# Kernel tuning notes

Measured on AMD Instinct MI355X. Metric: run time of the kernel, lower is better.

The kernel has to match this reference:

```python
import jax, jax.numpy as jnp
import numpy as np

B, S, D, H, HD = 8, 1374, 384, 6, 64
NUM_PATCHES = 1369  # (518 // 14) ** 2
NUM_PREFIX = 5      # 1 cls + 4 registers


def setup_inputs() -> dict:
    key = jax.random.key(0)
    ks = jax.random.split(key, 10)
    init = 0.02  # truncated_normal(0.02) approximated by scaled normal
    x = jax.random.normal(ks[0], (B, S, D), jnp.float32)
    wq = jax.random.truncated_normal(ks[1], -2.0, 2.0, (D, H, HD), jnp.float32) * init
    wk = jax.random.truncated_normal(ks[2], -2.0, 2.0, (D, H, HD), jnp.float32) * init
    wv = jax.random.truncated_normal(ks[3], -2.0, 2.0, (D, H, HD), jnp.float32) * init
    wo = jax.random.truncated_normal(ks[4], -2.0, 2.0, (H, HD, D), jnp.float32) * init
    bq = jnp.zeros((H, HD), jnp.float32)
    bk = jnp.zeros((H, HD), jnp.float32)
    bv = jnp.zeros((H, HD), jnp.float32)
    bo = jnp.zeros((D,), jnp.float32)
    keep_patch_indices = jax.random.randint(ks[5], (B, NUM_PATCHES), 0, NUM_PATCHES).astype(jnp.int64)
    return {"x": x, "wq": wq, "bq": bq, "wk": wk, "bk": bk, "wv": wv, "bv": bv,
            "wo": wo, "bo": bo, "keep_patch_indices": keep_patch_indices, "k_patches": 685}


def reference(x, wq, bq, wk, bk, wv, bv, wo, bo, keep_patch_indices, k_patches):
    # q/k/v projections: DenseGeneral to (heads, head_dim)
    q = jnp.einsum('bsd,dhe->bshe', x, wq) + bq
    k = jnp.einsum('bsd,dhe->bshe', x, wk) + bk
    v = jnp.einsum('bsd,dhe->bshe', x, wv) + bv

    z = jnp.einsum('bqhd,bkhd->bhqk', q / (HD ** 0.5), k)  # [B,H,S,S]
    attn_logits = z  # saved BEFORE masking (used by 'mse' criterion)

    # dynamic scatter mask: patch columns >= k_patches get -inf
    num_selected = keep_patch_indices.shape[1]
    patch_idx = jnp.arange(num_selected)
    indices_to_mask = jnp.where(patch_idx >= k_patches, patch_idx, num_selected) + NUM_PREFIX
    # out-of-bounds indices (== num_selected + NUM_PREFIX) are dropped by JAX scatter semantics
    z = z.at[:, :, :, indices_to_mask].set(-jnp.inf)

    attn_map = jax.nn.softmax(z, axis=-1)
    zo = jnp.einsum('bhqk,bkhd->bqhd', attn_map, v)
    output = jnp.einsum('bqhd,hdo->bqo', zo, wo) + bo  # wo contracts (heads, head_dim)

    # attn_aggregate = ['cls_token','reg_token','patch_token'], zoom_map_criterion='mse'
    am = attn_logits.mean(axis=1)  # mean over heads -> [B,S,S]
    aggs = jnp.stack([
        am[:, 0:1, :].mean(axis=1),      # cls token
        am[:, 1:5, :].mean(axis=1),      # register tokens
        am[:, 5:1374, :].mean(axis=1),   # patch tokens
    ], axis=1)                            # [B,3,S]
    attn_agg = aggs.mean(axis=1)          # [B,S]
    return output, attn_agg
```

## Files before the change

kernel.cpp:

```cpp
#include <hip/hip_runtime.h>
#include <stdint.h>

#define BB 8
#define SS 1374
#define DD 384
#define HH 6
#define HDIM 64
#define MROWS (BB*SS)
#define NPFX 5
#define SPAD 1376

typedef __attribute__((ext_vector_type(8))) short bf16x8;
typedef __attribute__((ext_vector_type(4))) float f32x4;
typedef __attribute__((ext_vector_type(2))) unsigned int u32x2;
typedef __attribute__((ext_vector_type(4))) unsigned int u32x4;
typedef u32x4 __attribute__((aligned(4))) u32x4_u;

__device__ __forceinline__ unsigned short f2bf(float f){
  union { float f; unsigned int u; } v; v.f = f;
  return (unsigned short)((v.u + 0x7FFFu + ((v.u >> 16) & 1u)) >> 16);
}
__device__ __forceinline__ float bf2f(unsigned short b){
  union { float f; unsigned int u; } v; v.u = ((unsigned int)b) << 16; return v.f;
}
__device__ __forceinline__ unsigned int pk_bf16(float a, float b){
#if __has_builtin(__builtin_amdgcn_cvt_pk_bf16_f32)
  typedef __attribute__((ext_vector_type(2))) __bf16 bfv2;
  bfv2 p = __builtin_amdgcn_cvt_pk_bf16_f32(a, b);
  union { bfv2 v; unsigned int u; } c; c.v = p; return c.u;
#else
  return (unsigned int)f2bf(a) | ((unsigned int)f2bf(b) << 16);
#endif
}

__global__ void k_conv_x(const float* __restrict__ x, unsigned short* __restrict__ xb, int n4){
  int i = blockIdx.x*blockDim.x + threadIdx.x;
  if (i >= n4) return;
  f32x4 v = *(const f32x4*)(x + (size_t)i*4);
  u32x2 o; o[0] = pk_bf16(v[0], v[1]); o[1] = pk_bf16(v[2], v[3]);
  *(u32x2*)(xb + (size_t)i*4) = o;
}

__global__ void k_conv_w(const float* __restrict__ wq, const float* __restrict__ wk,
                         const float* __restrict__ wv, const float* __restrict__ wo,
                         unsigned short* __restrict__ wbT, unsigned short* __restrict__ woT){
  int i = blockIdx.x*blockDim.x + threadIdx.x;
  if (i < 1152*384){
    int n = i / 384, d = i % 384;
    const float* w = (n < 384) ? wq : (n < 768) ? wk : wv;
    wbT[i] = f2bf(w[(size_t)d*384 + (n % 384)]);
  } else if (i < 1152*384 + 384*384){
    int j = i - 1152*384;
    int n = j / 384, k = j % 384;
    woT[j] = f2bf(wo[(size_t)k*384 + n]);
  }
}

__global__ void k_xbar(const float* __restrict__ x, float* __restrict__ xbar){
  int b = blockIdx.x / 11, ch = blockIdx.x % 11;
  int d = threadIdx.x;
  int s0 = ch*128, s1 = s0 + 128; if (s1 > SS) s1 = SS;
  float acc = 0.f;
  for (int s = s0; s < s1; ++s){
    float w = (s == 0) ? (1.f/3.f) : (s < 5) ? (1.f/12.f) : (1.f/4107.f);
    acc += w * x[((size_t)b*SS + s)*DD + d];
  }
  atomicAdd(&xbar[b*DD + d], acc);
}

__global__ void k_qbar(const float* __restrict__ xbar, const float* __restrict__ wq,
                       const float* __restrict__ bq, float* __restrict__ qbar){
  __shared__ float xs[DD];
  int b = blockIdx.x, t = threadIdx.x;
  xs[t] = xbar[b*DD + t];
  __syncthreads();
  float acc = bq[t];
  for (int d = 0; d < DD; ++d) acc += xs[d]*wq[(size_t)d*384 + t];
  qbar[b*384 + t] = acc;
}

__global__ void k_agg(const float* __restrict__ qbar, const unsigned short* __restrict__ kg,
                      float* __restrict__ out_agg){
  __shared__ float qs[384];
  int b = blockIdx.x / 6, sb = blockIdx.x % 6;
  int t = threadIdx.x;
  for (int i = t; i < 384; i += 256) qs[i] = qbar[b*384 + i];
  __syncthreads();
  int s = sb*256 + t;
  if (s >= SS) return;
  float acc = 0.f;
  for (int h = 0; h < HH; ++h){
    const unsigned short* kr = kg + (((size_t)(b*HH + h))*SS + s)*64;
    const float* qh = qs + h*64;
    for (int c = 0; c < 8; ++c){
      u32x4 v = *(const u32x4*)(kr + c*8);
      #pragma unroll
      for (int j = 0; j < 4; ++j){
        unsigned int u = v[j];
        acc += qh[c*8 + 2*j]     * bf2f((unsigned short)(u & 0xFFFFu));
        acc += qh[c*8 + 2*j + 1] * bf2f((unsigned short)(u >> 16));
      }
    }
  }
  out_agg[b*SS + s] = acc * (1.f/48.f);
}

template<int MODE>
__global__ __launch_bounds__(256) void k_gemm(
    const unsigned short* __restrict__ A, const unsigned short* __restrict__ Bt,
    const float* __restrict__ b0, const float* __restrict__ b1, const float* __restrict__ b2,
    unsigned short* __restrict__ qg, unsigned short* __restrict__ kgp,
    unsigned short* __restrict__ vt, float* __restrict__ out)
{
  int mt = blockIdx.x % 86, nt = blockIdx.x / 86;
  const int t = threadIdx.x;
  const int w = t >> 6, lane = t & 63, quad = lane >> 4, l16 = lane & 15;
  const int wm = w >> 1, wn = w & 1;
  constexpr int SMEM_SH = (MODE==0) ? 13824 : 17408;
  __shared__ unsigned short smem[SMEM_SH];
  unsigned short* As = smem;
  unsigned short* Bs = smem + 9216;
  f32x4 acc[4][2];
  #pragma unroll
  for (int i=0;i<4;i++){ acc[i][0] = (f32x4){0,0,0,0}; acc[i][1] = (f32x4){0,0,0,0}; }
  const int m0 = mt*128, n0 = nt*64;

  const int ar = t >> 1, akb = (t & 1) * 32;
  int ga = m0 + ar; if (ga > MROWS-1) ga = MROWS-1;
  const unsigned short* ap = A + (size_t)ga*384 + akb;
  const int br = t >> 2, bkb = (t & 3) * 16;
  const unsigned short* bp = Bt + (size_t)(n0 + br)*384 + bkb;

  u32x4 ra[4], rb[2];
  #pragma unroll
  for (int i=0;i<4;i++) ra[i] = *(const u32x4*)(ap + i*8);
  rb[0] = *(const u32x4*)(bp); rb[1] = *(const u32x4*)(bp + 8);

  for (int kc = 0; kc < 6; ++kc){
    __syncthreads();
    #pragma unroll
    for (int i=0;i<4;i++) *(u32x4*)(As + ar*72 + akb + i*8) = ra[i];
    *(u32x4*)(Bs + br*72 + bkb)     = rb[0];
    *(u32x4*)(Bs + br*72 + bkb + 8) = rb[1];
    __syncthreads();
    if (kc + 1 < 6){
      int kn = (kc+1)*64;
      #pragma unroll
      for (int i=0;i<4;i++) ra[i] = *(const u32x4*)(ap + kn + i*8);
      rb[0] = *(const u32x4*)(bp + kn); rb[1] = *(const u32x4*)(bp + kn + 8);
    }
    #pragma unroll
    for (int kh = 0; kh < 2; ++kh){
      bf16x8 af[4], bfr[2];
      #pragma unroll
      for (int rf = 0; rf < 4; ++rf)
        af[rf] = *(const bf16x8*)(As + (wm*64 + rf*16 + l16)*72 + kh*32 + quad*8);
      #pragma unroll
      for (int cf = 0; cf < 2; ++cf)
        bfr[cf] = *(const bf16x8*)(Bs + (wn*32 + cf*16 + l16)*72 + kh*32 + quad*8);
      #pragma unroll
      for (int rf = 0; rf < 4; ++rf)
        #pragma unroll
        for (int cf = 0; cf < 2; ++cf)
          acc[rf][cf] = __builtin_amdgcn_mfma_f32_16x16x32_bf16(af[rf], bfr[cf], acc[rf][cf], 0,0,0);
    }
  }

  const int b0r = m0 / SS, s0r = m0 % SS;
  __syncthreads();
  if (MODE == 1){
    float* CsF = (float*)smem;
    #pragma unroll
    for (int cf = 0; cf < 2; ++cf){
      int e = wn*32 + cf*16 + l16;
      float bias = b0[n0 + e];
      #pragma unroll
      for (int rf = 0; rf < 4; ++rf){
        int rr = wm*64 + rf*16 + quad*4;
        #pragma unroll
        for (int r4 = 0; r4 < 4; ++r4)
          CsF[(rr + r4)*68 + e] = acc[rf][cf][r4] + bias;
      }
    }
    __syncthreads();
    #pragma unroll
    for (int p = 0; p < 8; ++p){
      int r = p*16 + (t >> 4), c = t & 15;
      int rr = m0 + r;
      if (rr < MROWS){
        f32x4 v = *(const f32x4*)(CsF + r*68 + c*4);
        *(f32x4*)(out + (size_t)rr*384 + n0 + c*4) = v;
      }
    }
  } else {
    const int mat = nt / 6, h = nt - mat*6;
    const float* bvp = (mat==0) ? b0 : (mat==1) ? b1 : b2;
    const float vsc = (mat==0) ? 0.125f : 1.f;
    if (mat < 2){
      unsigned short* Cs = As;
      unsigned short* dst = (mat==0) ? qg : kgp;
      #pragma unroll
      for (int cf = 0; cf < 2; ++cf){
        int e = wn*32 + cf*16 + l16;
        float bias = bvp[h*64 + e];
        #pragma unroll
        for (int rf = 0; rf < 4; ++rf){
          int rr = wm*64 + rf*16 + quad*4;
          #pragma unroll
          for (int r4 = 0; r4 < 4; ++r4)
            Cs[(rr + r4)*72 + e] = f2bf((acc[rf][cf][r4] + bias)*vsc);
        }
      }
      __syncthreads();
      #pragma unroll
      for (int p = 0; p < 4; ++p){
        int r = p*32 + (t >> 3), c = t & 7;
        int rr = m0 + r;
        if (rr < MROWS){
          int s = s0r + r, bb = b0r;
          if (s >= SS){ s -= SS; ++bb; }
          u32x4 v = *(const u32x4*)(Cs + r*72 + c*8);
          *(u32x4*)(dst + (((size_t)(bb*HH + h))*SS + s)*64 + c*8) = v;
        }
      }
    } else {
      unsigned short* CsV = As;
      #pragma unroll
      for (int cf = 0; cf < 2; ++cf){
        int e = wn*32 + cf*16 + l16;
        float bias = bvp[h*64 + e];
        #pragma unroll
        for (int rf = 0; rf < 4; ++rf){
          int rr = wm*64 + rf*16 + quad*4;
          #pragma unroll
          for (int p = 0; p < 2; ++p)
            *(unsigned int*)(CsV + e*136 + rr + p*2) =
                pk_bf16(acc[rf][cf][p*2] + bias, acc[rf][cf][p*2+1] + bias);
        }
      }
      __syncthreads();
      const bool nowrap = (s0r + 127 < SS) && (m0 + 127 < MROWS);
      if (nowrap){
        int e = t >> 2;
        unsigned short* vrow = vt + ((size_t)(b0r*HH + h)*64 + e)*SPAD + s0r;
        #pragma unroll
        for (int i = 0; i < 4; ++i){
          int c = (t & 3)*4 + i;
          u32x4 v = *(const u32x4*)(CsV + e*136 + c*8);
          *(u32x4_u*)(vrow + c*8) = v;
        }
      } else {
        for (int idx = t; idx < 64*64; idx += 256){
          int e = idx >> 6, sp = (idx & 63)*2;
          int rr = m0 + sp;
          if (rr < MROWS){
            int s = s0r + sp, bb = b0r;
            if (s >= SS){ s -= SS; ++bb; }
            *(unsigned int*)(vt + ((size_t)(bb*HH + h)*64 + e)*SPAD + s) =
                *(const unsigned int*)(CsV + e*136 + sp);
          }
        }
      }
    }
  }
}

#define KSTR 72
__global__ __launch_bounds__(256) void k_attn(
    const unsigned short* __restrict__ qg, const unsigned short* __restrict__ kg,
    const unsigned short* __restrict__ vt, unsigned short* __restrict__ zo,
    const int* __restrict__ kpat)
{
  const int QB = (SS + 63)/64;
  int qb = blockIdx.x % QB, bh = blockIdx.x / QB;
  int t = threadIdx.x, w = t >> 6, lane = t & 63, quad = lane >> 4, l16 = lane & 15;
  int SK = NPFX + kpat[0]; if (SK > SS) SK = SS; if (SK < 1) SK = 1;
  int niter = (SK + 63) >> 6;
  __shared__ unsigned short Ks[64*KSTR];
  __shared__ unsigned short Vs[64*KSTR];
  __shared__ unsigned short Ps[4*16*KSTR];
  int q0 = qb*64 + w*16;
  bf16x8 aq[2];
  {
    int qrow = q0 + l16;
    if (qrow < SS){
      const unsigned short* p = qg + ((size_t)bh*SS + qrow)*64;
      aq[0] = *(const bf16x8*)(p + quad*8);
      aq[1] = *(const bf16x8*)(p + 32 + quad*8);
    } else {
      bf16x8 z8 = {0,0,0,0,0,0,0,0};
      aq[0] = z8; aq[1] = z8;
    }
  }
  f32x4 o[4];
  #pragma unroll
  for (int i=0;i<4;i++) o[i] = (f32x4){0.f,0.f,0.f,0.f};
  float rsum[4] = {0.f,0.f,0.f,0.f};

  const int srow = t >> 2, sc = t & 3;
  const unsigned short* kbase = kg + ((size_t)bh*SS)*64;
  const unsigned short* vbase = vt + ((size_t)bh*64)*SPAD;
  u32x4 rk0, rk1, rv0, rv1;
  rk0 = *(const u32x4*)(kbase + (size_t)srow*64 + sc*8);
  rk1 = *(const u32x4*)(kbase + (size_t)srow*64 + (sc+4)*8);
  rv0 = *(const u32x4*)(vbase + (size_t)srow*SPAD + sc*8);
  rv1 = *(const u32x4*)(vbase + (size_t)srow*SPAD + (sc+4)*8);

  for (int it = 0; it < niter; ++it){
    int k0 = it*64;
    __syncthreads();
    *(u32x4*)(Ks + srow*KSTR + sc*8)     = rk0;
    *(u32x4*)(Ks + srow*KSTR + (sc+4)*8) = rk1;
    *(u32x4*)(Vs + srow*KSTR + sc*8)     = rv0;
    *(u32x4*)(Vs + srow*KSTR + (sc+4)*8) = rv1;
    __syncthreads();
    if (it + 1 < niter){
      int kn = k0 + 64;
      rk0 = *(const u32x4*)(kbase + (size_t)(kn + srow)*64 + sc*8);
      rk1 = *(const u32x4*)(kbase + (size_t)(kn + srow)*64 + (sc+4)*8);
      rv0 = *(const u32x4*)(vbase + (size_t)srow*SPAD + kn + sc*8);
      rv1 = *(const u32x4*)(vbase + (size_t)srow*SPAD + kn + (sc+4)*8);
    }
    float p[2][2][4];
    bool tail = (k0 + 64 > SK);
    #pragma unroll
    for (int h = 0; h < 2; ++h){
      #pragma unroll
      for (int ns = 0; ns < 2; ++ns){
        f32x4 zf = (f32x4){0.f,0.f,0.f,0.f};
        #pragma unroll
        for (int ec = 0; ec < 2; ++ec){
          bf16x8 bkf = *(const bf16x8*)(Ks + (h*32 + 2*l16 + ns)*KSTR + ec*32 + quad*8);
          zf = __builtin_amdgcn_mfma_f32_16x16x32_bf16(aq[ec], bkf, zf, 0,0,0);
        }
        bool valid = !tail || (k0 + h*32 + 2*l16 + ns) < SK;
        #pragma unroll
        for (int rg = 0; rg < 4; ++rg) p[h][ns][rg] = valid ? __expf(zf[rg]) : 0.f;
      }
    }
    unsigned short* Pw = Ps + w*16*KSTR;
    #pragma unroll
    for (int rg = 0; rg < 4; ++rg){
      rsum[rg] += (p[0][0][rg] + p[0][1][rg]) + (p[1][0][rg] + p[1][1][rg]);
      *(unsigned int*)(Pw + (quad*4+rg)*KSTR      + 2*l16) = pk_bf16(p[0][0][rg], p[0][1][rg]);
      *(unsigned int*)(Pw + (quad*4+rg)*KSTR + 32 + 2*l16) = pk_bf16(p[1][0][rg], p[1][1][rg]);
    }
    #pragma unroll
    for (int kc = 0; kc < 2; ++kc){
      bf16x8 ap = *(const bf16x8*)(Pw + l16*KSTR + kc*32 + quad*8);
      #pragma unroll
      for (int nc = 0; nc < 4; ++nc){
        bf16x8 bvf = *(const bf16x8*)(Vs + (nc*16 + l16)*KSTR + kc*32 + quad*8);
        o[nc] = __builtin_amdgcn_mfma_f32_16x16x32_bf16(ap, bvf, o[nc], 0,0,0);
      }
    }
  }
  #pragma unroll
  for (int rg = 0; rg < 4; ++rg){
    float s = rsum[rg];
    #pragma unroll
    for (int off = 8; off >= 1; off >>= 1) s += __shfl_xor(s, off);
    rsum[rg] = s;
  }
  int b = bh / HH, h = bh % HH;
  #pragma unroll
  for (int rg = 0; rg < 4; ++rg){
    int q = q0 + quad*4 + rg;
    if (q >= SS) continue;
    float inv = 1.f / rsum[rg];
    unsigned short* dst = zo + ((size_t)b*SS + q)*384 + h*64;
    #pragma unroll
    for (int nc = 0; nc < 4; ++nc) dst[nc*16 + l16] = f2bf(o[nc][rg]*inv);
  }
}

extern "C" void kernel_launch(void* const* d_in, const int* in_sizes, int n_in,
                              void* d_out, int out_size, void* d_ws, size_t ws_size,
                              hipStream_t stream){
  const float* x  = (const float*)d_in[0];
  const float* wq = (const float*)d_in[1];
  const float* bq = (const float*)d_in[2];
  const float* wk = (const float*)d_in[3];
  const float* bk = (const float*)d_in[4];
  const float* wv = (const float*)d_in[5];
  const float* bv = (const float*)d_in[6];
  const float* wo = (const float*)d_in[7];
  const float* bo = (const float*)d_in[8];
  const int* kpat = (const int*)d_in[10];
  float* out = (float*)d_out;
  float* out_agg = out + (size_t)MROWS*DD;

  char* ws = (char*)d_ws;
  unsigned short* xb  = (unsigned short*)(ws);
  unsigned short* wbT = (unsigned short*)(ws +  8441856);
  unsigned short* woT = (unsigned short*)(ws +  9326592);
  unsigned short* qg  = (unsigned short*)(ws +  9621504);
  unsigned short* kg  = (unsigned short*)(ws + 18063360);
  unsigned short* vt  = (unsigned short*)(ws + 26505216);
  unsigned short* zo  = (unsigned short*)(ws + 34959360);
  float* xbar         = (float*)(ws + 43401216);
  float* qbar         = (float*)(ws + 43413504);
  (void)in_sizes; (void)n_in; (void)out_size; (void)ws_size;

  hipMemsetAsync(xbar, 0, BB*DD*sizeof(float), stream);
  k_conv_x<<<(MROWS*DD/4 + 255)/256, 256, 0, stream>>>(x, xb, MROWS*DD/4);
  k_conv_w<<<((1152*384 + 384*384) + 255)/256, 256, 0, stream>>>(wq, wk, wv, wo, wbT, woT);
  k_xbar<<<BB*11, DD, 0, stream>>>(x, xbar);
  k_qbar<<<BB, DD, 0, stream>>>(xbar, wq, bq, qbar);
  k_gemm<0><<<86*18, 256, 0, stream>>>(xb, wbT, bq, bk, bv, qg, kg, vt, nullptr);
  k_attn<<<BB*HH*22, 256, 0, stream>>>(qg, kg, vt, zo, kpat);
  k_agg<<<BB*6, 256, 0, stream>>>(qbar, kg, out_agg);
  k_gemm<1><<<86*6, 256, 0, stream>>>(zo, woT, bo, nullptr, nullptr, nullptr, nullptr, nullptr, out);
}
```

Measured before the change: 212.3 us.

## Fuse x conversion with xbar reduction; restructure attention to per-wave tiles without LDS staging

The x-to-bf16 conversion and the weighted xbar reduction now run in one kernel, so x is read from global memory once instead of twice. The attention kernel no longer stages K/V tiles through shared memory with block-wide barriers. Each wave handles 32 query rows as two 16-row fragments and loads K and V fragments straight from global memory, reusing each fragment across both query fragments. This removes the __syncthreads overhead and doubles register-level reuse per load. The cost is more global/L2 traffic per wave, since the four waves in a block no longer share K/V, and the scalar per-element bf16 stores in the fused prep kernel may be less efficient than the old vectorized conversion.

```diff
diff --git a/kernel.cpp b/kernel.cpp
--- a/kernel.cpp
+++ b/kernel.cpp
@@ -33,12 +33,19 @@
 #endif
 }
 
-__global__ void k_conv_x(const float* __restrict__ x, unsigned short* __restrict__ xb, int n4){
-  int i = blockIdx.x*blockDim.x + threadIdx.x;
-  if (i >= n4) return;
-  f32x4 v = *(const f32x4*)(x + (size_t)i*4);
-  u32x2 o; o[0] = pk_bf16(v[0], v[1]); o[1] = pk_bf16(v[2], v[3]);
-  *(u32x2*)(xb + (size_t)i*4) = o;
+__global__ void k_prep_x(const float* __restrict__ x, unsigned short* __restrict__ xb,
+                         float* __restrict__ xbar){
+  int b = blockIdx.x / 43, ch = blockIdx.x % 43;
+  int d = threadIdx.x;
+  int s0 = ch*32, s1 = s0 + 32; if (s1 > SS) s1 = SS;
+  float acc = 0.f;
+  for (int s = s0; s < s1; ++s){
+    float v = x[((size_t)b*SS + s)*DD + d];
+    float w = (s == 0) ? (1.f/3.f) : (s < 5) ? (1.f/12.f) : (1.f/4107.f);
+    acc += w * v;
+    xb[((size_t)b*SS + s)*DD + d] = f2bf(v);
+  }
+  atomicAdd(&xbar[b*DD + d], acc);
 }
 
 __global__ void k_conv_w(const float* __restrict__ wq, const float* __restrict__ wk,
@@ -54,18 +61,6 @@
     int n = j / 384, k = j % 384;
     woT[j] = f2bf(wo[(size_t)k*384 + n]);
   }
-}
-
-__global__ void k_xbar(const float* __restrict__ x, float* __restrict__ xbar){
-  int b = blockIdx.x / 11, ch = blockIdx.x % 11;
-  int d = threadIdx.x;
-  int s0 = ch*128, s1 = s0 + 128; if (s1 > SS) s1 = SS;
-  float acc = 0.f;
-  for (int s = s0; s < s1; ++s){
-    float w = (s == 0) ? (1.f/3.f) : (s < 5) ? (1.f/12.f) : (1.f/4107.f);
-    acc += w * x[((size_t)b*SS + s)*DD + d];
-  }
-  atomicAdd(&xbar[b*DD + d], acc);
 }
 
 __global__ void k_qbar(const float* __restrict__ xbar, const float* __restrict__ wq,
@@ -265,112 +260,96 @@
   }
 }
 
-#define KSTR 72
 __global__ __launch_bounds__(256) void k_attn(
     const unsigned short* __restrict__ qg, const unsigned short* __restrict__ kg,
     const unsigned short* __restrict__ vt, unsigned short* __restrict__ zo,
     const int* __restrict__ kpat)
 {
-  const int QB = (SS + 63)/64;
-  int qb = blockIdx.x % QB, bh = blockIdx.x / QB;
   int t = threadIdx.x, w = t >> 6, lane = t & 63, quad = lane >> 4, l16 = lane & 15;
+  int wid = blockIdx.x*4 + w;
+  int bh = wid / 43, qt = wid - bh*43;
+  int q0 = qt*32;
   int SK = NPFX + kpat[0]; if (SK > SS) SK = SS; if (SK < 1) SK = 1;
   int niter = (SK + 63) >> 6;
-  __shared__ unsigned short Ks[64*KSTR];
-  __shared__ unsigned short Vs[64*KSTR];
-  __shared__ unsigned short Ps[4*16*KSTR];
-  int q0 = qb*64 + w*16;
-  bf16x8 aq[2];
-  {
-    int qrow = q0 + l16;
-    if (qrow < SS){
-      const unsigned short* p = qg + ((size_t)bh*SS + qrow)*64;
-      aq[0] = *(const bf16x8*)(p + quad*8);
-      aq[1] = *(const bf16x8*)(p + 32 + quad*8);
-    } else {
-      bf16x8 z8 = {0,0,0,0,0,0,0,0};
-      aq[0] = z8; aq[1] = z8;
-    }
-  }
-  f32x4 o[4];
-  #pragma unroll
-  for (int i=0;i<4;i++) o[i] = (f32x4){0.f,0.f,0.f,0.f};
-  float rsum[4] = {0.f,0.f,0.f,0.f};
-
-  const int srow = t >> 2, sc = t & 3;
+  __shared__ unsigned short Ps[4][32*72];
+  unsigned short* Pw = &Ps[w][0];
   const unsigned short* kbase = kg + ((size_t)bh*SS)*64;
   const unsigned short* vbase = vt + ((size_t)bh*64)*SPAD;
-  u32x4 rk0, rk1, rv0, rv1;
-  rk0 = *(const u32x4*)(kbase + (size_t)srow*64 + sc*8);
-  rk1 = *(const u32x4*)(kbase + (size_t)srow*64 + (sc+4)*8);
-  rv0 = *(const u32x4*)(vbase + (size_t)srow*SPAD + sc*8);
-  rv1 = *(const u32x4*)(vbase + (size_t)srow*SPAD + (sc+4)*8);
+
+  bf16x8 aq[2][2];
+  #pragma unroll
+  for (int qf = 0; qf < 2; ++qf){
+    int qrow = q0 + qf*16 + l16; if (qrow > SS-1) qrow = SS-1;
+    const unsigned short* p = qg + ((size_t)bh*SS + qrow)*64;
+    aq[qf][0] = *(const bf16x8*)(p + quad*8);
+    aq[qf][1] = *(const bf16x8*)(p + 32 + quad*8);
+  }
+  f32x4 o[2][4];
+  #pragma unroll
+  for (int qf=0;qf<2;qf++)
+    #pragma unroll
+    for (int nc=0;nc<4;nc++) o[qf][nc] = (f32x4){0.f,0.f,0.f,0.f};
+  float rsum[2][4] = {{0.f,0.f,0.f,0.f},{0.f,0.f,0.f,0.f}};
 
   for (int it = 0; it < niter; ++it){
     int k0 = it*64;
-    __syncthreads();
-    *(u32x4*)(Ks + srow*KSTR + sc*8)     = rk0;
-    *(u32x4*)(Ks + srow*KSTR + (sc+4)*8) = rk1;
-    *(u32x4*)(Vs + srow*KSTR + sc*8)     = rv0;
-    *(u32x4*)(Vs + srow*KSTR + (sc+4)*8) = rv1;
-    __syncthreads();
-    if (it + 1 < niter){
-      int kn = k0 + 64;
-      rk0 = *(const u32x4*)(kbase + (size_t)(kn + srow)*64 + sc*8);
-      rk1 = *(const u32x4*)(kbase + (size_t)(kn + srow)*64 + (sc+4)*8);
-      rv0 = *(const u32x4*)(vbase + (size_t)srow*SPAD + kn + sc*8);
-      rv1 = *(const u32x4*)(vbase + (size_t)srow*SPAD + kn + (sc+4)*8);
-    }
-    float p[2][2][4];
     bool tail = (k0 + 64 > SK);
     #pragma unroll
-    for (int h = 0; h < 2; ++h){
+    for (int ks = 0; ks < 2; ++ks){
+      bf16x8 kf[2][2];
       #pragma unroll
       for (int ns = 0; ns < 2; ++ns){
-        f32x4 zf = (f32x4){0.f,0.f,0.f,0.f};
-        #pragma unroll
-        for (int ec = 0; ec < 2; ++ec){
-          bf16x8 bkf = *(const bf16x8*)(Ks + (h*32 + 2*l16 + ns)*KSTR + ec*32 + quad*8);
-          zf = __builtin_amdgcn_mfma_f32_16x16x32_bf16(aq[ec], bkf, zf, 0,0,0);
-        }
-        bool valid = !tail || (k0 + h*32 + 2*l16 + ns) < SK;
-        #pragma unroll
-        for (int rg = 0; rg < 4; ++rg) p[h][ns][rg] = valid ? __expf(zf[rg]) : 0.f;
-      }
-    }
-    unsigned short* Pw = Ps + w*16*KSTR;
+        const unsigned short* kr = kbase + (size_t)(k0 + ks*32 + 2*l16 + ns)*64;
+        kf[ns][0] = *(const bf16x8*)(kr + quad*8);
+        kf[ns][1] = *(const bf16x8*)(kr + 32 + quad*8);
+      }
+      #pragma unroll
+      for (int qf = 0; qf < 2; ++qf){
+        float pp[2][4];
+        #pragma unroll
+        for (int ns = 0; ns < 2; ++ns){
+          f32x4 zf = (f32x4){0.f,0.f,0.f,0.f};
+          zf = __builtin_amdgcn_mfma_f32_16x16x32_bf16(aq[qf][0], kf[ns][0], zf, 0,0,0);
+          zf = __builtin_amdgcn_mfma_f32_16x16x32_bf16(aq[qf][1], kf[ns][1], zf, 0,0,0);
+          bool valid = !tail || (k0 + ks*32 + 2*l16 + ns) < SK;
+          #pragma unroll
+          for (int rg = 0; rg < 4; ++rg) pp[ns][rg] = valid ? __expf(zf[rg]) : 0.f;
+        }
+        #pragma unroll
+        for (int rg = 0; rg < 4; ++rg){
+          rsum[qf][rg] += pp[0][rg] + pp[1][rg];
+          *(unsigned int*)(Pw + (qf*16 + quad*4 + rg)*72 + ks*32 + 2*l16) =
+              pk_bf16(pp[0][rg], pp[1][rg]);
+        }
+      }
+    }
+    #pragma unroll
+    for (int kc = 0; kc < 2; ++kc){
+      bf16x8 ap0 = *(const bf16x8*)(Pw + l16*72        + kc*32 + quad*8);
+      bf16x8 ap1 = *(const bf16x8*)(Pw + (16 + l16)*72 + kc*32 + quad*8);
+      #pragma unroll
+      for (int nc = 0; nc < 4; ++nc){
+        bf16x8 vf = *(const bf16x8*)(vbase + (size_t)(nc*16 + l16)*SPAD + k0 + kc*32 + quad*8);
+        o[0][nc] = __builtin_amdgcn_mfma_f32_16x16x32_bf16(ap0, vf, o[0][nc], 0,0,0);
+        o[1][nc] = __builtin_amdgcn_mfma_f32_16x16x32_bf16(ap1, vf, o[1][nc], 0,0,0);
+      }
+    }
+  }
+  int b = bh / HH, h = bh - (bh/HH)*HH;
+  #pragma unroll
+  for (int qf = 0; qf < 2; ++qf){
     #pragma unroll
     for (int rg = 0; rg < 4; ++rg){
-      rsum[rg] += (p[0][0][rg] + p[0][1][rg]) + (p[1][0][rg] + p[1][1][rg]);
-      *(unsigned int*)(Pw + (quad*4+rg)*KSTR      + 2*l16) = pk_bf16(p[0][0][rg], p[0][1][rg]);
-      *(unsigned int*)(Pw + (quad*4+rg)*KSTR + 32 + 2*l16) = pk_bf16(p[1][0][rg], p[1][1][rg]);
-    }
-    #pragma unroll
-    for (int kc = 0; kc < 2; ++kc){
-      bf16x8 ap = *(const bf16x8*)(Pw + l16*KSTR + kc*32 + quad*8);
-      #pragma unroll
-      for (int nc = 0; nc < 4; ++nc){
-        bf16x8 bvf = *(const bf16x8*)(Vs + (nc*16 + l16)*KSTR + kc*32 + quad*8);
-        o[nc] = __builtin_amdgcn_mfma_f32_16x16x32_bf16(ap, bvf, o[nc], 0,0,0);
-      }
-    }
-  }
-  #pragma unroll
-  for (int rg = 0; rg < 4; ++rg){
-    float s = rsum[rg];
-    #pragma unroll
-    for (int off = 8; off >= 1; off >>= 1) s += __shfl_xor(s, off);
-    rsum[rg] = s;
-  }
-  int b = bh / HH, h = bh % HH;
-  #pragma unroll
-  for (int rg = 0; rg < 4; ++rg){
-    int q = q0 + quad*4 + rg;
-    if (q >= SS) continue;
-    float inv = 1.f / rsum[rg];
-    unsigned short* dst = zo + ((size_t)b*SS + q)*384 + h*64;
-    #pragma unroll
-    for (int nc = 0; nc < 4; ++nc) dst[nc*16 + l16] = f2bf(o[nc][rg]*inv);
+      float s = rsum[qf][rg];
+      #pragma unroll
+      for (int off = 8; off >= 1; off >>= 1) s += __shfl_xor(s, off);
+      int q = q0 + qf*16 + quad*4 + rg;
+      if (q >= SS) continue;
+      float inv = 1.f / s;
+      unsigned short* dst = zo + ((size_t)b*SS + q)*384 + h*64;
+      #pragma unroll
+      for (int nc = 0; nc < 4; ++nc) dst[nc*16 + l16] = f2bf(o[qf][nc][rg]*inv);
+    }
   }
 }
 
@@ -403,12 +382,11 @@
   (void)in_sizes; (void)n_in; (void)out_size; (void)ws_size;
 
   hipMemsetAsync(xbar, 0, BB*DD*sizeof(float), stream);
-  k_conv_x<<<(MROWS*DD/4 + 255)/256, 256, 0, stream>>>(x, xb, MROWS*DD/4);
+  k_prep_x<<<BB*43, DD, 0, stream>>>(x, xb, xbar);
   k_conv_w<<<((1152*384 + 384*384) + 255)/256, 256, 0, stream>>>(wq, wk, wv, wo, wbT, woT);
-  k_xbar<<<BB*11, DD, 0, stream>>>(x, xbar);
   k_qbar<<<BB, DD, 0, stream>>>(xbar, wq, bq, qbar);
   k_gemm<0><<<86*18, 256, 0, stream>>>(xb, wbT, bq, bk, bv, qg, kg, vt, nullptr);
-  k_attn<<<BB*HH*22, 256, 0, stream>>>(qg, kg, vt, zo, kpat);
+  k_attn<<<516, 256, 0, stream>>>(qg, kg, vt, zo, kpat);
   k_agg<<<BB*6, 256, 0, stream>>>(qbar, kg, out_agg);
   k_gemm<1><<<86*6, 256, 0, stream>>>(zo, woT, bo, nullptr, nullptr, nullptr, nullptr, nullptr, out);
 }
```

Result: no change. 208.8 us (-1.7%).
